# Performance work log

Hardware: AMD Instinct MI355X
Metric: run time of the kernel (lower is better)

The kernel has to match this reference:

```python
import jax, jax.numpy as jnp
import numpy as np

B, T, D, H, OUT = 1024, 512, 6, 128, 8


def setup_inputs() -> dict:
    key = jax.random.key(0)
    ks = jax.random.split(key, 24)
    n = lambda k, shp, s=0.05: jax.random.normal(k, shp, dtype=jnp.float32) * s
    return {
        "src": jax.random.normal(ks[0], (B, T, D), dtype=jnp.float32),
        # pointwise conv stack (kernel size 1 -> plain matmuls)
        "w0": n(ks[1], (H, D)), "b0": n(ks[2], (H,)),
        "w1": n(ks[3], (H, H)), "b1": n(ks[4], (H,)),
        "w2": n(ks[5], (H, H)), "b2": n(ks[6], (H,)),
        "w3": n(ks[7], (H, H)), "b3": n(ks[8], (H,)),
        "pos_embed": n(ks[9], (T, 1, H)),
        # LSTM layer 0 (PyTorch gate order i,f,g,o stacked along dim 0)
        "Wih0": n(ks[10], (4 * H, H)), "Whh0": n(ks[11], (4 * H, H)),
        "bih0": n(ks[12], (4 * H,)), "bhh0": n(ks[13], (4 * H,)),
        # LSTM layer 1
        "Wih1": n(ks[14], (4 * H, H)), "Whh1": n(ks[15], (4 * H, H)),
        "bih1": n(ks[16], (4 * H,)), "bhh1": n(ks[17], (4 * H,)),
        # head: LayerNorm + Linear(H, H//4) + GELU + Linear(H//4, OUT)
        "ln_g": jnp.ones((H,), jnp.float32), "ln_b": jnp.zeros((H,), jnp.float32),
        "hw1": n(ks[18], (H // 4, H)), "hb1": n(ks[19], (H // 4,)),
        "hw2": n(ks[20], (OUT, H // 4)), "hb2": n(ks[21], (OUT,)),
    }


def _gelu(x):
    return jax.nn.gelu(x, approximate=False)  # torch default GELU (erf)


def _lstm_layer(xs, Wih, Whh, bih, bhh):
    # xs: (T, B, H) time-major; returns (all hidden states, final hidden state)
    Hd = Whh.shape[1]
    Bd = xs.shape[1]
    bias = bih + bhh
    h0 = jnp.zeros((Bd, Hd), xs.dtype)
    c0 = jnp.zeros((Bd, Hd), xs.dtype)

    def step(carry, x):
        h, c = carry
        z = x @ Wih.T + h @ Whh.T + bias  # (B, 4H)
        i, f, g, o = jnp.split(z, 4, axis=-1)
        c = jax.nn.sigmoid(f) * c + jax.nn.sigmoid(i) * jnp.tanh(g)
        h = jax.nn.sigmoid(o) * jnp.tanh(c)
        return (h, c), h

    (h, _), ys = jax.lax.scan(step, (h0, c0), xs)
    return ys, h


def reference(src, w0, b0, w1, b1, w2, b2, w3, b3, pos_embed,
              Wih0, Whh0, bih0, bhh0, Wih1, Whh1, bih1, bhh1,
              ln_g, ln_b, hw1, hb1, hw2, hb2):
    # pointwise Conv1d+GELU stack (kernel=1 -> per-timestep matmul), eval mode
    x = _gelu(src @ w0.T + b0)            # (B, T, H)
    x = _gelu(x @ w1.T + b1)
    x = _gelu(x @ w2.T + b2)
    x = _gelu(x @ w3.T + b3)
    x = jnp.transpose(x, (1, 0, 2)) + pos_embed  # (T, B, H), broadcast pos over batch
    ys, _ = _lstm_layer(x, Wih0, Whh0, bih0, bhh0)
    _, h = _lstm_layer(ys, Wih1, Whh1, bih1, bhh1)  # final hidden of last layer, (B, H)
    # head: LayerNorm (eps=1e-5) -> Linear -> GELU -> Linear (dropout inactive in eval)
    mu = h.mean(-1, keepdims=True)
    var = ((h - mu) ** 2).mean(-1, keepdims=True)
    hn = (h - mu) * jax.lax.rsqrt(var + 1e-5) * ln_g + ln_b
    return _gelu(hn @ hw1.T + hb1) @ hw2.T + hb2  # (B, OUT)
```

## Files before the change

kernel.cpp:

```cpp
#include <hip/hip_runtime.h>
#include <hip/hip_bf16.h>
#include <cstdint>

#define T_ 512
#define B_ 1024
#define D_ 6
#define H_ 128

typedef _Float16 f16;
typedef _Float16 f16x8 __attribute__((ext_vector_type(8)));
typedef float f32x4 __attribute__((ext_vector_type(4)));

__device__ __forceinline__ float erf_f(float x) {
    float ax = fabsf(x);
    float t = __builtin_amdgcn_rcpf(fmaf(0.3275911f, ax, 1.f));
    float p = fmaf(t, 1.061405429f, -1.453152027f);
    p = fmaf(t, p, 1.421413741f);
    p = fmaf(t, p, -0.284496736f);
    p = fmaf(t, p, 0.254829592f);
    p = p * t;
    float e = __builtin_amdgcn_exp2f(-ax * ax * 1.4426950408889634f);
    float r = 1.f - p * e;
    return copysignf(r, x);
}
__device__ __forceinline__ float gelu_f(float x) {
    return 0.5f * x * (1.f + erf_f(x * 0.7071067811865476f));
}
__device__ __forceinline__ float sig_f(float x) {
    return __builtin_amdgcn_rcpf(1.f + __builtin_amdgcn_exp2f(-1.4426950408889634f * x));
}
__device__ __forceinline__ float tanh_f(float x) {
    return 2.f * sig_f(2.f * x) - 1.f;
}
__device__ __forceinline__ f16x8 load8cvt(const float* p) {
    float4 a = ((const float4*)p)[0];
    float4 b = ((const float4*)p)[1];
    f16x8 r = { (f16)a.x, (f16)a.y, (f16)a.z, (f16)a.w,
                (f16)b.x, (f16)b.y, (f16)b.z, (f16)b.w };
    return r;
}
__device__ __forceinline__ f16x8 lds_rd8(const f16* base, int row, int cb) {
    const char* p = (const char*)base + row * 256 + (cb ^ ((row & 7) << 4));
    return *(const f16x8*)p;
}
__device__ __forceinline__ void lds_wr1(f16* base, int row, int col, f16 v) {
    char* p = (char*)base + row * 256 + ((col * 2) ^ ((row & 7) << 4));
    *(f16*)p = v;
}

__global__ __launch_bounds__(512, 2) void fused_conv_lstm0_k(
    const float* __restrict__ src,
    const float* __restrict__ w0p, const float* __restrict__ b0p,
    const float* __restrict__ w1p, const float* __restrict__ b1p,
    const float* __restrict__ w2p, const float* __restrict__ b2p,
    const float* __restrict__ w3p, const float* __restrict__ b3p,
    const float* __restrict__ posp,
    const float* __restrict__ Wih, const float* __restrict__ Whh,
    const float* __restrict__ bih, const float* __restrict__ bhh,
    f16* __restrict__ ys)
{
    __shared__ f16 CW[3 * 8 * 4 * 512];
    __shared__ f16 XA[16 * 128];
    __shared__ f16 XB[16 * 128];
    __shared__ f16 HL[2][16 * 128];
    const int tid = threadIdx.x;
    const int lane = tid & 63, wid = tid >> 6;
    const int l16 = lane & 15, hi = lane >> 4;
    const int bb0 = blockIdx.x * 4;
    const int mycol = wid * 16 + l16;

    f16x8 wih[4][4], whh[4][4];
    float biasg[4];
#pragma unroll
    for (int g = 0; g < 4; ++g) {
        int n = g * 128 + mycol;
        biasg[g] = bih[n] + bhh[n];
#pragma unroll
        for (int ki = 0; ki < 4; ++ki) {
            wih[g][ki] = load8cvt(Wih + n * 128 + ki * 32 + hi * 8);
            whh[g][ki] = load8cvt(Whh + n * 128 + ki * 32 + hi * 8);
        }
    }

    const int col0 = tid & 127;
    const int row0 = tid >> 7;
    float w0c[6], b0c;
#pragma unroll
    for (int k = 0; k < 6; ++k) w0c[k] = w0p[col0 * 6 + k];
    b0c = b0p[col0];
    const float b1c = b1p[mycol], b2c = b2p[mycol], b3c = b3p[mycol];

    {
        const float* wp[3] = { w1p, w2p, w3p };
        for (int i = tid; i < 6144; i += 512) {
            int ln = i & 63, ki = (i >> 6) & 3, cg = (i >> 8) & 7, L = i >> 11;
            f16x8 v = load8cvt(wp[L] + (cg * 16 + (ln & 15)) * 128 + ki * 32 + (ln >> 4) * 8);
            *(f16x8*)(CW + i * 8) = v;
        }
    }
    for (int i = tid; i < 2 * 16 * 128; i += 512) ((f16*)HL)[i] = (f16)0.f;

    float sv[6];
    {
        const float2* sp = (const float2*)src + ((size_t)(bb0 + row0) * T_) * 3;
        float2 a = sp[0], b = sp[1], c2 = sp[2];
        sv[0] = a.x; sv[1] = a.y; sv[2] = b.x; sv[3] = b.y; sv[4] = c2.x; sv[5] = c2.y;
    }
    float c = 0.f, h = 0.f;
    __syncthreads();

    auto conv_layer = [&](const f16* Xin, f16* Xout, int L, float bc, float addv) {
        f16x8 af[4], bf[4];
#pragma unroll
        for (int ki = 0; ki < 4; ++ki) {
            af[ki] = lds_rd8(Xin, l16, ki * 64 + hi * 16);
            bf[ki] = *(const f16x8*)(CW + (((L * 8 + wid) * 4 + ki) << 9) + lane * 8);
        }
        f32x4 acc = { bc, bc, bc, bc };
#pragma unroll
        for (int ki = 0; ki < 4; ++ki)
            acc = __builtin_amdgcn_mfma_f32_16x16x32_f16(af[ki], bf[ki], acc, 0, 0, 0);
        lds_wr1(Xout, hi * 4, mycol, (f16)(gelu_f(acc[0]) + addv));
    };

    for (int t = 0; t < T_; ++t) {
        {
            float a = b0c;
#pragma unroll
            for (int k = 0; k < 6; ++k) a = fmaf(sv[k], w0c[k], a);
            lds_wr1(XA, row0 * 4, col0, (f16)gelu_f(a));
        }
        if (wid == 0 && t > 0) {
            f16x8 v = lds_rd8(HL[t & 1], (lane >> 4) * 4, (lane & 15) * 16);
            *(f16x8*)(ys + (size_t)(t - 1) * (B_ * H_) +
                      (size_t)(bb0 + (lane >> 4)) * H_ + (lane & 15) * 8) = v;
        }
        const float pv = posp[t * 128 + mycol];
        float svn[6];
        {
            const int tn = (t + 1 < T_) ? t + 1 : t;
            const float2* sp = (const float2*)src + ((size_t)(bb0 + row0) * T_ + tn) * 3;
            float2 a = sp[0], b = sp[1], c2 = sp[2];
            svn[0] = a.x; svn[1] = a.y; svn[2] = b.x; svn[3] = b.y; svn[4] = c2.x; svn[5] = c2.y;
        }
        __syncthreads();
        conv_layer(XA, XB, 0, b1c, 0.f);
        __syncthreads();
        conv_layer(XB, XA, 1, b2c, 0.f);
        __syncthreads();
        conv_layer(XA, XB, 2, b3c, pv);
        __syncthreads();
        {
            f16x8 xa[4], ha[4];
#pragma unroll
            for (int ki = 0; ki < 4; ++ki) {
                xa[ki] = lds_rd8(XB, l16, ki * 64 + hi * 16);
                ha[ki] = lds_rd8(HL[t & 1], l16, ki * 64 + hi * 16);
            }
            f32x4 acc[4];
#pragma unroll
            for (int g = 0; g < 4; ++g) {
                f32x4 bv = { biasg[g], biasg[g], biasg[g], biasg[g] };
                acc[g] = bv;
            }
#pragma unroll
            for (int ki = 0; ki < 4; ++ki)
#pragma unroll
                for (int g = 0; g < 4; ++g)
                    acc[g] = __builtin_amdgcn_mfma_f32_16x16x32_f16(xa[ki], wih[g][ki], acc[g], 0, 0, 0);
#pragma unroll
            for (int ki = 0; ki < 4; ++ki)
#pragma unroll
                for (int g = 0; g < 4; ++g)
                    acc[g] = __builtin_amdgcn_mfma_f32_16x16x32_f16(ha[ki], whh[g][ki], acc[g], 0, 0, 0);
            float zi = acc[0][0], zf = acc[1][0], zg = acc[2][0], zo = acc[3][0];
            c = sig_f(zf) * c + sig_f(zi) * tanh_f(zg);
            h = sig_f(zo) * tanh_f(c);
            lds_wr1(HL[(t + 1) & 1], hi * 4, mycol, (f16)h);
        }
#pragma unroll
        for (int k = 0; k < 6; ++k) sv[k] = svn[k];
        __syncthreads();
    }
    if (wid == 0) {
        f16x8 v = lds_rd8(HL[0], (lane >> 4) * 4, (lane & 15) * 16);
        *(f16x8*)(ys + (size_t)(T_ - 1) * (B_ * H_) +
                  (size_t)(bb0 + (lane >> 4)) * H_ + (lane & 15) * 8) = v;
    }
}

__global__ __launch_bounds__(512, 2) void lstm1_k(
    const f16* __restrict__ xb,
    const float* __restrict__ Wih, const float* __restrict__ Whh,
    const float* __restrict__ bih, const float* __restrict__ bhh,
    float* __restrict__ hfin)
{
    __shared__ f16 HL[2][16 * 128];
    const int tid = threadIdx.x;
    const int lane = tid & 63, wid = tid >> 6;
    const int l16 = lane & 15, hi = lane >> 4;
    const int bb0 = blockIdx.x * 4;

    f16x8 wih[4][4], whh[4][4];
    float bias[4];
#pragma unroll
    for (int g = 0; g < 4; ++g) {
        int n = g * 128 + wid * 16 + l16;
        bias[g] = bih[n] + bhh[n];
#pragma unroll
        for (int ki = 0; ki < 4; ++ki) {
            wih[g][ki] = load8cvt(Wih + n * 128 + ki * 32 + hi * 8);
            whh[g][ki] = load8cvt(Whh + n * 128 + ki * 32 + hi * 8);
        }
    }
    for (int i = tid; i < 2 * 16 * 128; i += 512) ((f16*)HL)[i] = (f16)0.f;

    const bool arow = (l16 & 3) == 0;
    const int brow = l16 >> 2;
    const f16* xbase = xb + (size_t)(bb0 + brow) * H_;
    const int mycol = wid * 16 + l16;
    float c = 0.f, h = 0.f;
    __syncthreads();

    f16x8 xa[4];
    const f16x8 zero8 = { 0, 0, 0, 0, 0, 0, 0, 0 };
#pragma unroll
    for (int ki = 0; ki < 4; ++ki)
        xa[ki] = arow ? *(const f16x8*)(xbase + ki * 32 + hi * 8) : zero8;

    for (int t = 0; t < T_; ++t) {
        const int tn = (t + 1 < T_) ? t + 1 : T_ - 1;
        const f16* xnp = xbase + (size_t)tn * (B_ * H_);
        f16x8 xn[4];
#pragma unroll
        for (int ki = 0; ki < 4; ++ki)
            xn[ki] = arow ? *(const f16x8*)(xnp + ki * 32 + hi * 8) : zero8;

        f16x8 ha[4];
#pragma unroll
        for (int ki = 0; ki < 4; ++ki)
            ha[ki] = lds_rd8(HL[t & 1], l16, ki * 64 + hi * 16);

        f32x4 acc[4];
#pragma unroll
        for (int g = 0; g < 4; ++g) {
            f32x4 bv = { bias[g], bias[g], bias[g], bias[g] };
            acc[g] = bv;
        }
#pragma unroll
        for (int ki = 0; ki < 4; ++ki)
#pragma unroll
            for (int g = 0; g < 4; ++g)
                acc[g] = __builtin_amdgcn_mfma_f32_16x16x32_f16(xa[ki], wih[g][ki], acc[g], 0, 0, 0);
#pragma unroll
        for (int ki = 0; ki < 4; ++ki)
#pragma unroll
            for (int g = 0; g < 4; ++g)
                acc[g] = __builtin_amdgcn_mfma_f32_16x16x32_f16(ha[ki], whh[g][ki], acc[g], 0, 0, 0);

        float zi = acc[0][0], zf = acc[1][0], zg = acc[2][0], zo = acc[3][0];
        c = sig_f(zf) * c + sig_f(zi) * tanh_f(zg);
        h = sig_f(zo) * tanh_f(c);
        lds_wr1(HL[(t + 1) & 1], hi * 4, mycol, (f16)h);

#pragma unroll
        for (int ki = 0; ki < 4; ++ki) xa[ki] = xn[ki];
        __syncthreads();
    }
    hfin[(size_t)(bb0 + hi) * H_ + mycol] = h;
}

__global__ __launch_bounds__(256) void head_k(
    const float* __restrict__ hfin,
    const float* __restrict__ lng, const float* __restrict__ lnb,
    const float* __restrict__ hw1, const float* __restrict__ hb1,
    const float* __restrict__ hw2, const float* __restrict__ hb2,
    float* __restrict__ outp)
{
    __shared__ float HN[4][128];
    __shared__ float G[4][32];
    const int tid = threadIdx.x, lane = tid & 63, wid = tid >> 6;
    const int b = blockIdx.x * 4 + wid;
    float v0 = hfin[b * 128 + lane], v1 = hfin[b * 128 + 64 + lane];
    float s = v0 + v1;
#pragma unroll
    for (int m = 1; m < 64; m <<= 1) s += __shfl_xor(s, m);
    float mu = s * (1.f / 128.f);
    float d0 = v0 - mu, d1 = v1 - mu;
    float q = d0 * d0 + d1 * d1;
#pragma unroll
    for (int m = 1; m < 64; m <<= 1) q += __shfl_xor(q, m);
    float rs = rsqrtf(q * (1.f / 128.f) + 1e-5f);
    HN[wid][lane] = d0 * rs * lng[lane] + lnb[lane];
    HN[wid][64 + lane] = d1 * rs * lng[64 + lane] + lnb[64 + lane];
    __syncthreads();
    if (tid < 128) {
        int row = tid >> 5, o = tid & 31;
        float a = hb1[o];
#pragma unroll 4
        for (int k = 0; k < 128; ++k) a = fmaf(HN[row][k], hw1[o * 128 + k], a);
        G[row][o] = gelu_f(a);
    }
    __syncthreads();
    if (tid < 32) {
        int row = tid >> 3, oo = tid & 7;
        float a = hb2[oo];
#pragma unroll
        for (int k = 0; k < 32; ++k) a = fmaf(G[row][k], hw2[oo * 32 + k], a);
        outp[(size_t)(blockIdx.x * 4 + row) * 8 + oo] = a;
    }
}

extern "C" void kernel_launch(void* const* d_in, const int* in_sizes, int n_in,
                              void* d_out, int out_size, void* d_ws, size_t ws_size,
                              hipStream_t stream) {
    (void)in_sizes; (void)n_in; (void)out_size; (void)ws_size;
    const float* src  = (const float*)d_in[0];
    const float* w0   = (const float*)d_in[1];
    const float* b0   = (const float*)d_in[2];
    const float* w1   = (const float*)d_in[3];
    const float* b1   = (const float*)d_in[4];
    const float* w2   = (const float*)d_in[5];
    const float* b2   = (const float*)d_in[6];
    const float* w3   = (const float*)d_in[7];
    const float* b3   = (const float*)d_in[8];
    const float* pos  = (const float*)d_in[9];
    const float* Wih0 = (const float*)d_in[10];
    const float* Whh0 = (const float*)d_in[11];
    const float* bih0 = (const float*)d_in[12];
    const float* bhh0 = (const float*)d_in[13];
    const float* Wih1 = (const float*)d_in[14];
    const float* Whh1 = (const float*)d_in[15];
    const float* bih1 = (const float*)d_in[16];
    const float* bhh1 = (const float*)d_in[17];
    const float* lng  = (const float*)d_in[18];
    const float* lnb  = (const float*)d_in[19];
    const float* hw1  = (const float*)d_in[20];
    const float* hb1  = (const float*)d_in[21];
    const float* hw2  = (const float*)d_in[22];
    const float* hb2  = (const float*)d_in[23];
    float* outp = (float*)d_out;

    f16* ysbuf = (f16*)d_ws;
    float* hfin = (float*)((char*)d_ws + (size_t)134217728);

    fused_conv_lstm0_k<<<dim3(256), dim3(512), 0, stream>>>(
        src, w0, b0, w1, b1, w2, b2, w3, b3, pos,
        Wih0, Whh0, bih0, bhh0, ysbuf);
    lstm1_k<<<dim3(256), dim3(512), 0, stream>>>(
        ysbuf, Wih1, Whh1, bih1, bhh1, hfin);
    head_k<<<dim3(256), dim3(256), 0, stream>>>(
        hfin, lng, lnb, hw1, hb1, hw2, hb2, outp);
}
```

Baseline: 1.319 ms.

## Chunk conv stack and input projection over 8 timesteps in fused LSTM0 kernel

```diff
diff --git a/kernel.cpp b/kernel.cpp
--- a/kernel.cpp
+++ b/kernel.cpp
@@ -6,6 +6,7 @@
 #define B_ 1024
 #define D_ 6
 #define H_ 128
+#define CH_ 8
 
 typedef _Float16 f16;
 typedef _Float16 f16x8 __attribute__((ext_vector_type(8)));
@@ -46,6 +47,14 @@
 __device__ __forceinline__ void lds_wr1(f16* base, int row, int col, f16 v) {
     char* p = (char*)base + row * 256 + ((col * 2) ^ ((row & 7) << 4));
     *(f16*)p = v;
+}
+__device__ __forceinline__ void zx_wr(f16* base, int row, int col, f16 v) {
+    char* p = (char*)base + row * 1024 + ((col * 2) ^ ((row & 7) << 4));
+    *(f16*)p = v;
+}
+__device__ __forceinline__ float zx_rd(const f16* base, int row, int col) {
+    const char* p = (const char*)base + row * 1024 + ((col * 2) ^ ((row & 7) << 4));
+    return (float)*(const f16*)p;
 }
 
 __global__ __launch_bounds__(512, 2) void fused_conv_lstm0_k(
@@ -60,30 +69,38 @@
     f16* __restrict__ ys)
 {
     __shared__ f16 CW[3 * 8 * 4 * 512];
-    __shared__ f16 XA[16 * 128];
-    __shared__ f16 XB[16 * 128];
-    __shared__ f16 HL[2][16 * 128];
+    __shared__ f16 XA0[32 * 128];
+    __shared__ f16 XA1[32 * 128];
+    __shared__ f16 ZX[32 * 512];
+    __shared__ f16 YH[32 * 128];
+    __shared__ f16 HL[2][4 * 128];
+
     const int tid = threadIdx.x;
     const int lane = tid & 63, wid = tid >> 6;
     const int l16 = lane & 15, hi = lane >> 4;
     const int bb0 = blockIdx.x * 4;
     const int mycol = wid * 16 + l16;
 
-    f16x8 wih[4][4], whh[4][4];
+    f16x8 whh[4][4], wxg[4][4];
     float biasg[4];
 #pragma unroll
     for (int g = 0; g < 4; ++g) {
         int n = g * 128 + mycol;
         biasg[g] = bih[n] + bhh[n];
 #pragma unroll
-        for (int ki = 0; ki < 4; ++ki) {
-            wih[g][ki] = load8cvt(Wih + n * 128 + ki * 32 + hi * 8);
+        for (int ki = 0; ki < 4; ++ki)
             whh[g][ki] = load8cvt(Whh + n * 128 + ki * 32 + hi * 8);
-        }
+    }
+#pragma unroll
+    for (int nt = 0; nt < 4; ++nt) {
+        int n = wid * 64 + nt * 16 + l16;
+#pragma unroll
+        for (int ki = 0; ki < 4; ++ki)
+            wxg[nt][ki] = load8cvt(Wih + n * 128 + ki * 32 + hi * 8);
     }
 
     const int col0 = tid & 127;
-    const int row0 = tid >> 7;
+    const int r0 = tid >> 7;
     float w0c[6], b0c;
 #pragma unroll
     for (int k = 0; k < 6; ++k) w0c[k] = w0p[col0 * 6 + k];
@@ -98,65 +115,95 @@
             *(f16x8*)(CW + i * 8) = v;
         }
     }
-    for (int i = tid; i < 2 * 16 * 128; i += 512) ((f16*)HL)[i] = (f16)0.f;
-
-    float sv[6];
-    {
-        const float2* sp = (const float2*)src + ((size_t)(bb0 + row0) * T_) * 3;
-        float2 a = sp[0], b = sp[1], c2 = sp[2];
-        sv[0] = a.x; sv[1] = a.y; sv[2] = b.x; sv[3] = b.y; sv[4] = c2.x; sv[5] = c2.y;
-    }
+    for (int i = tid; i < 2 * 4 * 128; i += 512) ((f16*)HL)[i] = (f16)0.f;
+
     float c = 0.f, h = 0.f;
     __syncthreads();
 
-    auto conv_layer = [&](const f16* Xin, f16* Xout, int L, float bc, float addv) {
-        f16x8 af[4], bf[4];
-#pragma unroll
-        for (int ki = 0; ki < 4; ++ki) {
-            af[ki] = lds_rd8(Xin, l16, ki * 64 + hi * 16);
+    auto conv_mfma = [&](const f16* Xin, f16* Xout, int L, float bc, int t0pos) {
+        f16x8 bf[4];
+#pragma unroll
+        for (int ki = 0; ki < 4; ++ki)
             bf[ki] = *(const f16x8*)(CW + (((L * 8 + wid) * 4 + ki) << 9) + lane * 8);
-        }
-        f32x4 acc = { bc, bc, bc, bc };
-#pragma unroll
-        for (int ki = 0; ki < 4; ++ki)
-            acc = __builtin_amdgcn_mfma_f32_16x16x32_f16(af[ki], bf[ki], acc, 0, 0, 0);
-        lds_wr1(Xout, hi * 4, mycol, (f16)(gelu_f(acc[0]) + addv));
+#pragma unroll
+        for (int mt = 0; mt < 2; ++mt) {
+            f16x8 af[4];
+#pragma unroll
+            for (int ki = 0; ki < 4; ++ki)
+                af[ki] = lds_rd8(Xin, mt * 16 + l16, ki * 64 + hi * 16);
+            f32x4 acc = { bc, bc, bc, bc };
+#pragma unroll
+            for (int ki = 0; ki < 4; ++ki)
+                acc = __builtin_amdgcn_mfma_f32_16x16x32_f16(af[ki], bf[ki], acc, 0, 0, 0);
+            float pv = 0.f;
+            if (t0pos >= 0) pv = posp[(t0pos + mt * 4 + hi) * 128 + mycol];
+#pragma unroll
+            for (int j = 0; j < 4; ++j)
+                lds_wr1(Xout, mt * 16 + hi * 4 + j, mycol, (f16)(gelu_f(acc[j]) + pv));
+        }
     };
 
-    for (int t = 0; t < T_; ++t) {
+    auto flushYH = [&](int tc) {
+        int tau = tid >> 4, cw = tid & 15;
+        f16x8 v = lds_rd8(YH, tau, cw * 16);
+        *(f16x8*)(ys + (size_t)(tc + (tau >> 2)) * (B_ * H_) +
+                  (size_t)(bb0 + (tau & 3)) * H_ + cw * 8) = v;
+    };
+
+    for (int t0 = 0; t0 < T_; t0 += CH_) {
         {
-            float a = b0c;
-#pragma unroll
-            for (int k = 0; k < 6; ++k) a = fmaf(sv[k], w0c[k], a);
-            lds_wr1(XA, row0 * 4, col0, (f16)gelu_f(a));
-        }
-        if (wid == 0 && t > 0) {
-            f16x8 v = lds_rd8(HL[t & 1], (lane >> 4) * 4, (lane & 15) * 16);
-            *(f16x8*)(ys + (size_t)(t - 1) * (B_ * H_) +
-                      (size_t)(bb0 + (lane >> 4)) * H_ + (lane & 15) * 8) = v;
-        }
-        const float pv = posp[t * 128 + mycol];
-        float svn[6];
-        {
-            const int tn = (t + 1 < T_) ? t + 1 : t;
-            const float2* sp = (const float2*)src + ((size_t)(bb0 + row0) * T_ + tn) * 3;
-            float2 a = sp[0], b = sp[1], c2 = sp[2];
-            svn[0] = a.x; svn[1] = a.y; svn[2] = b.x; svn[3] = b.y; svn[4] = c2.x; svn[5] = c2.y;
-        }
-        __syncthreads();
-        conv_layer(XA, XB, 0, b1c, 0.f);
-        __syncthreads();
-        conv_layer(XB, XA, 1, b2c, 0.f);
-        __syncthreads();
-        conv_layer(XA, XB, 2, b3c, pv);
-        __syncthreads();
-        {
-            f16x8 xa[4], ha[4];
-#pragma unroll
-            for (int ki = 0; ki < 4; ++ki) {
-                xa[ki] = lds_rd8(XB, l16, ki * 64 + hi * 16);
-                ha[ki] = lds_rd8(HL[t & 1], l16, ki * 64 + hi * 16);
+            const float2* sp0 = (const float2*)src + ((size_t)(bb0 + r0) * T_ + t0) * 3;
+#pragma unroll
+            for (int it = 0; it < CH_; ++it) {
+                float2 a = sp0[it * 3 + 0], b = sp0[it * 3 + 1], c2 = sp0[it * 3 + 2];
+                float acc = b0c;
+                acc = fmaf(a.x, w0c[0], acc);
+                acc = fmaf(a.y, w0c[1], acc);
+                acc = fmaf(b.x, w0c[2], acc);
+                acc = fmaf(b.y, w0c[3], acc);
+                acc = fmaf(c2.x, w0c[4], acc);
+                acc = fmaf(c2.y, w0c[5], acc);
+                lds_wr1(XA0, it * 4 + r0, col0, (f16)gelu_f(acc));
             }
+        }
+        if (t0 > 0) flushYH(t0 - CH_);
+        __syncthreads();
+        conv_mfma(XA0, XA1, 0, b1c, -1);
+        __syncthreads();
+        conv_mfma(XA1, XA0, 1, b2c, -1);
+        __syncthreads();
+        conv_mfma(XA0, XA1, 2, b3c, t0);
+        __syncthreads();
+#pragma unroll
+        for (int mt = 0; mt < 2; ++mt) {
+            f16x8 af[4];
+#pragma unroll
+            for (int ki = 0; ki < 4; ++ki)
+                af[ki] = lds_rd8(XA1, mt * 16 + l16, ki * 64 + hi * 16);
+            f32x4 za[4];
+#pragma unroll
+            for (int nt = 0; nt < 4; ++nt) {
+                f32x4 zz = { 0.f, 0.f, 0.f, 0.f };
+                za[nt] = zz;
+            }
+#pragma unroll
+            for (int ki = 0; ki < 4; ++ki)
+#pragma unroll
+                for (int nt = 0; nt < 4; ++nt)
+                    za[nt] = __builtin_amdgcn_mfma_f32_16x16x32_f16(af[ki], wxg[nt][ki], za[nt], 0, 0, 0);
+#pragma unroll
+            for (int nt = 0; nt < 4; ++nt)
+#pragma unroll
+                for (int j = 0; j < 4; ++j)
+                    zx_wr(ZX, mt * 16 + hi * 4 + j, wid * 64 + nt * 16 + l16, (f16)za[nt][j]);
+        }
+        __syncthreads();
+        for (int it = 0; it < CH_; ++it) {
+            const int t = t0 + it;
+            f16x8 ha[4];
+#pragma unroll
+            for (int ki = 0; ki < 4; ++ki)
+                ha[ki] = lds_rd8(HL[t & 1], l16 >> 2, ki * 64 + hi * 16);
             f32x4 acc[4];
 #pragma unroll
             for (int g = 0; g < 4; ++g) {
@@ -167,26 +214,19 @@
             for (int ki = 0; ki < 4; ++ki)
 #pragma unroll
                 for (int g = 0; g < 4; ++g)
-                    acc[g] = __builtin_amdgcn_mfma_f32_16x16x32_f16(xa[ki], wih[g][ki], acc[g], 0, 0, 0);
-#pragma unroll
-            for (int ki = 0; ki < 4; ++ki)
-#pragma unroll
-                for (int g = 0; g < 4; ++g)
                     acc[g] = __builtin_amdgcn_mfma_f32_16x16x32_f16(ha[ki], whh[g][ki], acc[g], 0, 0, 0);
-            float zi = acc[0][0], zf = acc[1][0], zg = acc[2][0], zo = acc[3][0];
+            float zi = acc[0][0] + zx_rd(ZX, it * 4 + hi, 0 + mycol);
+            float zf = acc[1][0] + zx_rd(ZX, it * 4 + hi, 128 + mycol);
+            float zg = acc[2][0] + zx_rd(ZX, it * 4 + hi, 256 + mycol);
+            float zo = acc[3][0] + zx_rd(ZX, it * 4 + hi, 384 + mycol);
             c = sig_f(zf) * c + sig_f(zi) * tanh_f(zg);
             h = sig_f(zo) * tanh_f(c);
-            lds_wr1(HL[(t + 1) & 1], hi * 4, mycol, (f16)h);
-        }
-#pragma unroll
-        for (int k = 0; k < 6; ++k) sv[k] = svn[k];
-        __syncthreads();
-    }
-    if (wid == 0) {
-        f16x8 v = lds_rd8(HL[0], (lane >> 4) * 4, (lane & 15) * 16);
-        *(f16x8*)(ys + (size_t)(T_ - 1) * (B_ * H_) +
-                  (size_t)(bb0 + (lane >> 4)) * H_ + (lane & 15) * 8) = v;
-    }
+            lds_wr1(HL[(t + 1) & 1], hi, mycol, (f16)h);
+            lds_wr1(YH, it * 4 + hi, mycol, (f16)h);
+            __syncthreads();
+        }
+    }
+    flushYH(T_ - CH_);
 }
 
 __global__ __launch_bounds__(512, 2) void lstm1_k(
```

New measurement: 1.639 ms. 24.2% more time.
